# Optimization experiments

Measured on AMD Instinct MI355X. Metric: run time of the kernel, lower is better.

Reference implementation:

```python
import jax, jax.numpy as jnp
import numpy as np

D_MODEL = 256
N_BINS = 11
# standard KNRM kernels: exact-match bin (mu=1, sigma=1e-3) + 10 soft bins
MUS = jnp.array([1.0, 0.9, 0.7, 0.5, 0.3, 0.1, -0.1, -0.3, -0.5, -0.7, -0.9], dtype=jnp.float32)
SIGMAS = jnp.array([1e-3] + [0.1] * 10, dtype=jnp.float32)


def _l2norm(x, eps=1e-10):
    # F.normalize(p=2, eps=1e-10): x / max(||x||, eps)
    n = jnp.sqrt(jnp.sum(x * x, axis=-1, keepdims=True))
    return x / jnp.maximum(n, eps)


def setup_inputs() -> dict:
    key = jax.random.key(0)
    ks = jax.random.split(key, 10)
    B, NB, Q, T, D = 64, 8, 32, 256, D_MODEL
    return {
        "word_atten": jax.random.uniform(ks[0], (B, NB, Q), dtype=jnp.float32),
        "hq": jax.random.normal(ks[1], (B, NB, Q, D), dtype=jnp.float32),
        "can": jax.random.normal(ks[2], (B, T, D), dtype=jnp.float32),
        "rep": jax.random.normal(ks[3], (B, NB, D), dtype=jnp.float32),
        "rep_cur": jax.random.normal(ks[4], (B, D), dtype=jnp.float32),
        "mask_hq": jnp.ones((B, NB, Q), dtype=jnp.float32),
        "mask_can": jnp.ones((B, T), dtype=jnp.float32),
        "mask_session": jnp.ones((B, NB), dtype=jnp.float32),
        "W_dense": jax.random.normal(ks[5], (N_BINS, 1), dtype=jnp.float32) * 0.3,
        "b_dense": jnp.zeros((1,), dtype=jnp.float32),
        "W_att": jax.random.normal(ks[6], (D, D), dtype=jnp.float32) * (1.0 / np.sqrt(D)),
        "b_att": jnp.zeros((D,), dtype=jnp.float32),
    }


def reference(word_atten, hq, can, rep, rep_cur, mask_hq, mask_can, mask_session,
              W_dense, b_dense, W_att, b_att):
    # cosine-similarity matrix: [B, NB, Q, T]
    hq_n = _l2norm(hq)
    can_n = _l2norm(can)
    matrix = jnp.einsum("bnqd,btd->bnqt", hq_n, can_n)

    # Gaussian kernel soft-binning: expand to [B, NB, Q, T, N_BINS]
    diff = matrix[..., None] - MUS  # broadcast over bins
    kern = jnp.exp(-(diff * diff) / (2.0 * SIGMAS * SIGMAS))
    kern = kern * mask_can[:, None, None, :, None]  # mask doc tokens
    pooling_sum = jnp.sum(kern, axis=3)  # [B, NB, Q, N_BINS]

    log_pool = jnp.log(jnp.clip(pooling_sum, 1e-10)) * 0.01
    log_pool = log_pool * mask_hq[..., None] * word_atten[..., None]
    pooled = jnp.sum(log_pool, axis=2)  # [B, NB, N_BINS]

    pooled = pooled * mask_session[..., None]

    # attention over session blocks (AttendAttention): scaled dot with projected current rep
    q = rep_cur @ W_att + b_att  # [B, D]
    scores = jnp.einsum("bnd,bd->bn", rep, q) / np.sqrt(D_MODEL).astype(np.float32)
    scores = jnp.where(mask_session > 0, scores, -1e9)
    attn = jax.nn.softmax(scores, axis=-1)  # [B, NB]

    score = jnp.tanh(pooled @ W_dense + b_dense).squeeze(-1)  # [B, NB]
    return jnp.sum(score * attn, axis=1)  # [B]
```

## Files before the change

kernel.cpp:

```cpp
#include <hip/hip_runtime.h>

#define B_ 64
#define NB_ 8
#define Q_ 32
#define T_ 256
#define D_ 256
#define NBINS 11

typedef __attribute__((ext_vector_type(8))) short bf16x8;
typedef __attribute__((ext_vector_type(4))) float f32x4;
typedef unsigned short ushort_t;
typedef unsigned int uint_t;

__device__ inline ushort_t bf16_rnd(float f) {
  uint_t u = __float_as_uint(f);
  return (ushort_t)((u + 0x8000u) >> 16);
}
__device__ inline uint_t pack2(ushort_t a, ushort_t b) {
  return (uint_t)a | ((uint_t)b << 16);
}

__global__ __launch_bounds__(256) void pool_kernel(
    const float* __restrict__ hq, const float* __restrict__ can,
    const float* __restrict__ mask_can, float* __restrict__ psum) {
  __shared__ __align__(16) ushort_t can_hi[32 * 264];
  __shared__ __align__(16) ushort_t can_lo[32 * 264];
  float* partial = (float*)can_hi;

  const float mus[NBINS] = {1.0f, 0.9f, 0.7f, 0.5f, 0.3f, 0.1f,
                            -0.1f, -0.3f, -0.5f, -0.7f, -0.9f};
  const float nis2[NBINS] = {-5.0e5f, -50.f, -50.f, -50.f, -50.f, -50.f,
                             -50.f, -50.f, -50.f, -50.f, -50.f};

  int i = blockIdx.x;
  int b = i & 63;
  int nb = (i >> 6) & 7;
  int th = i >> 9;
  int outb = b * NB_ + nb;
  int tid = threadIdx.x;
  int wv = tid >> 6, lane = tid & 63;
  int lq = lane & 15, lk = lane >> 4;
  int mtile = wv >> 1, ntile = wv & 1;

  const float* hq_base = hq + (size_t)outb * (Q_ * D_);
  const float* can_base = can + (size_t)b * (T_ * D_);
  const float* maskcan_b = mask_can + b * T_;

  const float* arow = hq_base + (size_t)(mtile * 16 + lq) * D_;
  float sumsq = 0.f;
#pragma unroll
  for (int kk = 0; kk < 8; kk++) {
    const float* p = arow + kk * 32 + lk * 8;
    float4 x = reinterpret_cast<const float4*>(p)[0];
    float4 y = reinterpret_cast<const float4*>(p)[1];
    sumsq += x.x * x.x + x.y * x.y + x.z * x.z + x.w * x.w +
             y.x * y.x + y.y * y.y + y.z * y.z + y.w * y.w;
  }
  sumsq += __shfl_xor(sumsq, 16);
  sumsq += __shfl_xor(sumsq, 32);
  float ainv = 1.0f / fmaxf(sqrtf(sumsq), 1e-10f);

  bf16x8 a_hi[8], a_lo[8];
#pragma unroll
  for (int kk = 0; kk < 8; kk++) {
    const float* p = arow + kk * 32 + lk * 8;
    float4 x = reinterpret_cast<const float4*>(p)[0];
    float4 y = reinterpret_cast<const float4*>(p)[1];
    float v[8] = {x.x, x.y, x.z, x.w, y.x, y.y, y.z, y.w};
    union { bf16x8 v8; ushort_t u[8]; } H, L;
#pragma unroll
    for (int j = 0; j < 8; j++) {
      float s = v[j] * ainv;
      ushort_t h = bf16_rnd(s);
      float hf = __uint_as_float(((uint_t)h) << 16);
      H.u[j] = h;
      L.u[j] = bf16_rnd(s - hf);
    }
    a_hi[kk] = H.v8;
    a_lo[kk] = L.v8;
  }

  float binacc[4][NBINS];
#pragma unroll
  for (int r = 0; r < 4; r++)
#pragma unroll
    for (int j = 0; j < NBINS; j++) binacc[r][j] = 0.0f;

  for (int ch = 0; ch < 4; ch++) {
    __syncthreads();
#pragma unroll
    for (int it = 0; it < 4; it++) {
      int flat = it * 2048 + tid * 8;
      int row = flat >> 8, col = flat & 255;
      int trow = th * 128 + ch * 32 + row;
      const float* src = can_base + (size_t)trow * D_ + col;
      float4 x = reinterpret_cast<const float4*>(src)[0];
      float4 y = reinterpret_cast<const float4*>(src)[1];
      float s = x.x * x.x + x.y * x.y + x.z * x.z + x.w * x.w +
                y.x * y.x + y.y * y.y + y.z * y.z + y.w * y.w;
      s += __shfl_xor(s, 1);
      s += __shfl_xor(s, 2);
      s += __shfl_xor(s, 4);
      s += __shfl_xor(s, 8);
      s += __shfl_xor(s, 16);
      float inv = 1.0f / fmaxf(sqrtf(s), 1e-10f);
      float v[8] = {x.x, x.y, x.z, x.w, y.x, y.y, y.z, y.w};
      ushort_t h[8], l[8];
#pragma unroll
      for (int j = 0; j < 8; j++) {
        float sv = v[j] * inv;
        h[j] = bf16_rnd(sv);
        float hf = __uint_as_float(((uint_t)h[j]) << 16);
        l[j] = bf16_rnd(sv - hf);
      }
      uint4 ph = {pack2(h[0], h[1]), pack2(h[2], h[3]), pack2(h[4], h[5]),
                  pack2(h[6], h[7])};
      uint4 pl = {pack2(l[0], l[1]), pack2(l[2], l[3]), pack2(l[4], l[5]),
                  pack2(l[6], l[7])};
      *reinterpret_cast<uint4*>(&can_hi[row * 264 + col]) = ph;
      *reinterpret_cast<uint4*>(&can_lo[row * 264 + col]) = pl;
    }
    __syncthreads();

    f32x4 acc = {0.f, 0.f, 0.f, 0.f};
    const ushort_t* Bhi = &can_hi[(ntile * 16 + lq) * 264];
    const ushort_t* Blo = &can_lo[(ntile * 16 + lq) * 264];
#pragma unroll
    for (int kk = 0; kk < 8; kk++) {
      int off = kk * 32 + lk * 8;
      bf16x8 bh = *reinterpret_cast<const bf16x8*>(Bhi + off);
      bf16x8 bl = *reinterpret_cast<const bf16x8*>(Blo + off);
      acc = __builtin_amdgcn_mfma_f32_16x16x32_bf16(a_hi[kk], bh, acc, 0, 0, 0);
      acc = __builtin_amdgcn_mfma_f32_16x16x32_bf16(a_lo[kk], bh, acc, 0, 0, 0);
      acc = __builtin_amdgcn_mfma_f32_16x16x32_bf16(a_hi[kk], bl, acc, 0, 0, 0);
    }

    int t0 = th * 128 + ch * 32 + ntile * 16 + lq;
    float mk = maskcan_b[t0];
#pragma unroll
    for (int r = 0; r < 4; r++) {
      float v0 = acc[r];
#pragma unroll
      for (int j = 0; j < NBINS; j++) {
        float d0 = v0 - mus[j];
        binacc[r][j] += mk * __expf(d0 * d0 * nis2[j]);
      }
    }
  }

  __syncthreads();

#pragma unroll
  for (int r = 0; r < 4; r++)
#pragma unroll
    for (int j = 0; j < NBINS; j++) {
      float v = binacc[r][j];
      v += __shfl_xor(v, 1);
      v += __shfl_xor(v, 2);
      v += __shfl_xor(v, 4);
      v += __shfl_xor(v, 8);
      binacc[r][j] = v;
    }
  if (lq == 0) {
#pragma unroll
    for (int r = 0; r < 4; r++)
#pragma unroll
      for (int j = 0; j < NBINS; j++)
        partial[(wv * 16 + lk * 4 + r) * NBINS + j] = binacc[r][j];
  }
  __syncthreads();

  float* dst = &psum[(size_t)(outb * 2 + th) * (Q_ * NBINS)];
  for (int idx = tid; idx < Q_ * NBINS; idx += 256) {
    int q = idx / NBINS;
    int j = idx - q * NBINS;
    int mt = q >> 4, lr = q & 15;
    dst[idx] = partial[((2 * mt) * 16 + lr) * NBINS + j] +
               partial[((2 * mt + 1) * 16 + lr) * NBINS + j];
  }
}

__global__ __launch_bounds__(256) void final_kernel(
    const float* __restrict__ rep, const float* __restrict__ rep_cur,
    const float* __restrict__ mask_session, const float* __restrict__ W_dense,
    const float* __restrict__ b_dense, const float* __restrict__ W_att,
    const float* __restrict__ b_att, const float* __restrict__ word_atten,
    const float* __restrict__ mask_hq, const float* __restrict__ psum,
    float* __restrict__ out) {
  __shared__ float lp[NB_ * Q_ * NBINS];
  __shared__ float pooled_sm[NB_ * NBINS];
  __shared__ float qproj[D_];
  __shared__ float scores_sm[NB_];
  int b = blockIdx.x, tid = threadIdx.x;

  {
    int nb = tid >> 5, q = tid & 31;
    int outb = b * NB_ + nb;
    float wa = word_atten[outb * Q_ + q] * mask_hq[outb * Q_ + q];
    const float* p0 = &psum[(size_t)(outb * 2 + 0) * (Q_ * NBINS) + q * NBINS];
    const float* p1 = &psum[(size_t)(outb * 2 + 1) * (Q_ * NBINS) + q * NBINS];
#pragma unroll
    for (int j = 0; j < NBINS; j++) {
      float s = p0[j] + p1[j];
      lp[(nb * Q_ + q) * NBINS + j] = logf(fmaxf(s, 1e-10f)) * 0.01f * wa;
    }
  }

  const float* rc = rep_cur + b * D_;
  float acc = b_att[tid];
  for (int k = 0; k < D_; k++) acc += rc[k] * W_att[k * D_ + tid];
  qproj[tid] = acc;
  __syncthreads();

  if (tid < NB_ * NBINS) {
    int nb = tid / NBINS, j = tid - nb * NBINS;
    float s = 0.f;
#pragma unroll
    for (int q = 0; q < Q_; q++) s += lp[(nb * Q_ + q) * NBINS + j];
    pooled_sm[nb * NBINS + j] = s;
  }

  int wv = tid >> 6, lane = tid & 63;
  for (int nn = wv; nn < NB_; nn += 4) {
    const float* rp = rep + ((size_t)b * NB_ + nn) * D_;
    float4 r4 = reinterpret_cast<const float4*>(rp)[lane];
    float4 q4 = *reinterpret_cast<float4*>(&qproj[lane * 4]);
    float s = r4.x * q4.x + r4.y * q4.y + r4.z * q4.z + r4.w * q4.w;
#pragma unroll
    for (int off = 32; off > 0; off >>= 1) s += __shfl_down(s, off);
    if (lane == 0) scores_sm[nn] = s * 0.0625f;
  }
  __syncthreads();

  if (tid == 0) {
    float sc[NB_];
    float mx = -1e30f;
    for (int nn = 0; nn < NB_; nn++) {
      float s = (mask_session[b * NB_ + nn] > 0.f) ? scores_sm[nn] : -1e9f;
      sc[nn] = s;
      mx = fmaxf(mx, s);
    }
    float den = 0.f;
    for (int nn = 0; nn < NB_; nn++) {
      sc[nn] = __expf(sc[nn] - mx);
      den += sc[nn];
    }
    float res = 0.f;
    for (int nn = 0; nn < NB_; nn++) {
      float ms = mask_session[b * NB_ + nn];
      float pw = b_dense[0];
      for (int j = 0; j < NBINS; j++)
        pw += pooled_sm[nn * NBINS + j] * ms * W_dense[j];
      res += tanhf(pw) * (sc[nn] / den);
    }
    out[b] = res;
  }
}

extern "C" void kernel_launch(void* const* d_in, const int* in_sizes, int n_in,
                              void* d_out, int out_size, void* d_ws,
                              size_t ws_size, hipStream_t stream) {
  const float* word_atten = (const float*)d_in[0];
  const float* hq = (const float*)d_in[1];
  const float* can = (const float*)d_in[2];
  const float* rep = (const float*)d_in[3];
  const float* rep_cur = (const float*)d_in[4];
  const float* mask_hq = (const float*)d_in[5];
  const float* mask_can = (const float*)d_in[6];
  const float* mask_session = (const float*)d_in[7];
  const float* W_dense = (const float*)d_in[8];
  const float* b_dense = (const float*)d_in[9];
  const float* W_att = (const float*)d_in[10];
  const float* b_att = (const float*)d_in[11];
  float* out = (float*)d_out;

  float* psum = (float*)d_ws;

  hipLaunchKernelGGL(pool_kernel, dim3(1024), dim3(256), 0, stream, hq, can,
                     mask_can, psum);
  hipLaunchKernelGGL(final_kernel, dim3(B_), dim3(256), 0, stream, rep,
                     rep_cur, mask_session, W_dense, b_dense, W_att, b_att,
                     word_atten, mask_hq, psum, out);
}
```

Before: 151.6 us.

## Precompute normalized bf16 hi/lo operand tiles in separate kernel, pipeline pool MFMA loop

Adds a split_kernel that normalizes can and hq once and writes bf16 hi/lo halves to workspace, already arranged in the MFMA fragment layout. Previously each pool block re-normalized and re-split the can rows, and that work was repeated for every nb. pool_kernel now loads fragments straight from global memory with no shared staging and no barriers. It uses 512 blocks that each cover all T, and overlaps the next tile's loads and MFMAs with the exp binning of the previous tile. The cost is an extra launch, a round trip of the converted data through global memory, and more registers, capped by launch_bounds(256,2).

```diff
diff --git a/kernel.cpp b/kernel.cpp
--- a/kernel.cpp
+++ b/kernel.cpp
@@ -12,6 +12,12 @@
 typedef unsigned short ushort_t;
 typedef unsigned int uint_t;
 
+#define CANH_OFF 0u
+#define CANL_OFF 8388608u
+#define HQH_OFF 16777216u
+#define HQL_OFF 25165824u
+#define PSUM_OFF 33554432u
+
 __device__ inline ushort_t bf16_rnd(float f) {
   uint_t u = __float_as_uint(f);
   return (ushort_t)((u + 0x8000u) >> 16);
@@ -20,12 +26,80 @@
   return (uint_t)a | ((uint_t)b << 16);
 }
 
-__global__ __launch_bounds__(256) void pool_kernel(
-    const float* __restrict__ hq, const float* __restrict__ can,
+__global__ __launch_bounds__(256) void split_kernel(
+    const float* __restrict__ can, const float* __restrict__ hq,
+    uint4* __restrict__ canH, uint4* __restrict__ canL,
+    uint4* __restrict__ hqH, uint4* __restrict__ hqL) {
+  __shared__ __align__(16) ushort_t sm_hi[32 * 264];
+  __shared__ __align__(16) ushort_t sm_lo[32 * 264];
+  int blk = blockIdx.x;
+  int tid = threadIdx.x;
+  const float* src;
+  uint4 *dH, *dL;
+  int tilebase;
+  if (blk < 512) {
+    int b = blk >> 3, ch = blk & 7;
+    src = can + ((size_t)b * T_ + ch * 32) * D_;
+    tilebase = b * 16 + ch * 2;
+    dH = canH;
+    dL = canL;
+  } else {
+    int outb = blk - 512;
+    src = hq + (size_t)outb * Q_ * D_;
+    tilebase = outb * 2;
+    dH = hqH;
+    dL = hqL;
+  }
+#pragma unroll
+  for (int it = 0; it < 4; it++) {
+    int flat = it * 2048 + tid * 8;
+    int row = flat >> 8, col = flat & 255;
+    const float* p = src + row * D_ + col;
+    float4 x = reinterpret_cast<const float4*>(p)[0];
+    float4 y = reinterpret_cast<const float4*>(p)[1];
+    float s = x.x * x.x + x.y * x.y + x.z * x.z + x.w * x.w +
+              y.x * y.x + y.y * y.y + y.z * y.z + y.w * y.w;
+    s += __shfl_xor(s, 1);
+    s += __shfl_xor(s, 2);
+    s += __shfl_xor(s, 4);
+    s += __shfl_xor(s, 8);
+    s += __shfl_xor(s, 16);
+    float inv = 1.0f / fmaxf(sqrtf(s), 1e-10f);
+    float v[8] = {x.x, x.y, x.z, x.w, y.x, y.y, y.z, y.w};
+    ushort_t h[8], l[8];
+#pragma unroll
+    for (int j = 0; j < 8; j++) {
+      float sv = v[j] * inv;
+      h[j] = bf16_rnd(sv);
+      float hf = __uint_as_float(((uint_t)h[j]) << 16);
+      l[j] = bf16_rnd(sv - hf);
+    }
+    uint4 ph = {pack2(h[0], h[1]), pack2(h[2], h[3]), pack2(h[4], h[5]),
+                pack2(h[6], h[7])};
+    uint4 pl = {pack2(l[0], l[1]), pack2(l[2], l[3]), pack2(l[4], l[5]),
+                pack2(l[6], l[7])};
+    *reinterpret_cast<uint4*>(&sm_hi[row * 264 + col]) = ph;
+    *reinterpret_cast<uint4*>(&sm_lo[row * 264 + col]) = pl;
+  }
+  __syncthreads();
+  int wv = tid >> 6, lane = tid & 63;
+  int tl = wv >> 1, part = wv & 1;
+  int lq = lane & 15, lk = lane >> 4;
+  const ushort_t* smp = part ? sm_lo : sm_hi;
+  uint4* dst = part ? dL : dH;
+#pragma unroll
+  for (int kk = 0; kk < 8; kk++) {
+    const ushort_t* a = &smp[(tl * 16 + lq) * 264 + kk * 32 + lk * 8];
+    dst[((size_t)(tilebase + tl) * 8 + kk) * 64 + lane] =
+        *reinterpret_cast<const uint4*>(a);
+  }
+}
+
+__global__ __launch_bounds__(256, 2) void pool_kernel(
+    const uint4* __restrict__ canH, const uint4* __restrict__ canL,
+    const uint4* __restrict__ hqH, const uint4* __restrict__ hqL,
     const float* __restrict__ mask_can, float* __restrict__ psum) {
-  __shared__ __align__(16) ushort_t can_hi[32 * 264];
-  __shared__ __align__(16) ushort_t can_lo[32 * 264];
-  float* partial = (float*)can_hi;
+  __shared__ float partial[4 * 16 * NBINS];
 
   const float mus[NBINS] = {1.0f, 0.9f, 0.7f, 0.5f, 0.3f, 0.1f,
                             -0.1f, -0.3f, -0.5f, -0.7f, -0.9f};
@@ -34,50 +108,21 @@
 
   int i = blockIdx.x;
   int b = i & 63;
-  int nb = (i >> 6) & 7;
-  int th = i >> 9;
+  int nb = i >> 6;
   int outb = b * NB_ + nb;
   int tid = threadIdx.x;
   int wv = tid >> 6, lane = tid & 63;
   int lq = lane & 15, lk = lane >> 4;
-  int mtile = wv >> 1, ntile = wv & 1;
-
-  const float* hq_base = hq + (size_t)outb * (Q_ * D_);
-  const float* can_base = can + (size_t)b * (T_ * D_);
-  const float* maskcan_b = mask_can + b * T_;
-
-  const float* arow = hq_base + (size_t)(mtile * 16 + lq) * D_;
-  float sumsq = 0.f;
-#pragma unroll
-  for (int kk = 0; kk < 8; kk++) {
-    const float* p = arow + kk * 32 + lk * 8;
-    float4 x = reinterpret_cast<const float4*>(p)[0];
-    float4 y = reinterpret_cast<const float4*>(p)[1];
-    sumsq += x.x * x.x + x.y * x.y + x.z * x.z + x.w * x.w +
-             y.x * y.x + y.y * y.y + y.z * y.z + y.w * y.w;
-  }
-  sumsq += __shfl_xor(sumsq, 16);
-  sumsq += __shfl_xor(sumsq, 32);
-  float ainv = 1.0f / fmaxf(sqrtf(sumsq), 1e-10f);
-
-  bf16x8 a_hi[8], a_lo[8];
-#pragma unroll
-  for (int kk = 0; kk < 8; kk++) {
-    const float* p = arow + kk * 32 + lk * 8;
-    float4 x = reinterpret_cast<const float4*>(p)[0];
-    float4 y = reinterpret_cast<const float4*>(p)[1];
-    float v[8] = {x.x, x.y, x.z, x.w, y.x, y.y, y.z, y.w};
-    union { bf16x8 v8; ushort_t u[8]; } H, L;
-#pragma unroll
-    for (int j = 0; j < 8; j++) {
-      float s = v[j] * ainv;
-      ushort_t h = bf16_rnd(s);
-      float hf = __uint_as_float(((uint_t)h) << 16);
-      H.u[j] = h;
-      L.u[j] = bf16_rnd(s - hf);
-    }
-    a_hi[kk] = H.v8;
-    a_lo[kk] = L.v8;
+  int mtile = wv & 1, tq = wv >> 1;
+
+  bf16x8 ah[8], al[8];
+  {
+    size_t abase = (size_t)(outb * 2 + mtile) * 8 * 64 + lane;
+#pragma unroll
+    for (int kk = 0; kk < 8; kk++) {
+      ah[kk] = *reinterpret_cast<const bf16x8*>(&hqH[abase + kk * 64]);
+      al[kk] = *reinterpret_cast<const bf16x8*>(&hqL[abase + kk * 64]);
+    }
   }
 
   float binacc[4][NBINS];
@@ -86,69 +131,62 @@
 #pragma unroll
     for (int j = 0; j < NBINS; j++) binacc[r][j] = 0.0f;
 
-  for (int ch = 0; ch < 4; ch++) {
-    __syncthreads();
-#pragma unroll
-    for (int it = 0; it < 4; it++) {
-      int flat = it * 2048 + tid * 8;
-      int row = flat >> 8, col = flat & 255;
-      int trow = th * 128 + ch * 32 + row;
-      const float* src = can_base + (size_t)trow * D_ + col;
-      float4 x = reinterpret_cast<const float4*>(src)[0];
-      float4 y = reinterpret_cast<const float4*>(src)[1];
-      float s = x.x * x.x + x.y * x.y + x.z * x.z + x.w * x.w +
-                y.x * y.x + y.y * y.y + y.z * y.z + y.w * y.w;
-      s += __shfl_xor(s, 1);
-      s += __shfl_xor(s, 2);
-      s += __shfl_xor(s, 4);
-      s += __shfl_xor(s, 8);
-      s += __shfl_xor(s, 16);
-      float inv = 1.0f / fmaxf(sqrtf(s), 1e-10f);
-      float v[8] = {x.x, x.y, x.z, x.w, y.x, y.y, y.z, y.w};
-      ushort_t h[8], l[8];
-#pragma unroll
-      for (int j = 0; j < 8; j++) {
-        float sv = v[j] * inv;
-        h[j] = bf16_rnd(sv);
-        float hf = __uint_as_float(((uint_t)h[j]) << 16);
-        l[j] = bf16_rnd(sv - hf);
-      }
-      uint4 ph = {pack2(h[0], h[1]), pack2(h[2], h[3]), pack2(h[4], h[5]),
-                  pack2(h[6], h[7])};
-      uint4 pl = {pack2(l[0], l[1]), pack2(l[2], l[3]), pack2(l[4], l[5]),
-                  pack2(l[6], l[7])};
-      *reinterpret_cast<uint4*>(&can_hi[row * 264 + col]) = ph;
-      *reinterpret_cast<uint4*>(&can_lo[row * 264 + col]) = pl;
-    }
-    __syncthreads();
-
+  f32x4 accPrev;
+  float mkPrev = 0.0f;
+
+  {
+    int tt = tq * 8;
+    size_t bbase = (size_t)(b * 16 + tt) * 8 * 64 + lane;
     f32x4 acc = {0.f, 0.f, 0.f, 0.f};
-    const ushort_t* Bhi = &can_hi[(ntile * 16 + lq) * 264];
-    const ushort_t* Blo = &can_lo[(ntile * 16 + lq) * 264];
 #pragma unroll
     for (int kk = 0; kk < 8; kk++) {
-      int off = kk * 32 + lk * 8;
-      bf16x8 bh = *reinterpret_cast<const bf16x8*>(Bhi + off);
-      bf16x8 bl = *reinterpret_cast<const bf16x8*>(Blo + off);
-      acc = __builtin_amdgcn_mfma_f32_16x16x32_bf16(a_hi[kk], bh, acc, 0, 0, 0);
-      acc = __builtin_amdgcn_mfma_f32_16x16x32_bf16(a_lo[kk], bh, acc, 0, 0, 0);
-      acc = __builtin_amdgcn_mfma_f32_16x16x32_bf16(a_hi[kk], bl, acc, 0, 0, 0);
-    }
-
-    int t0 = th * 128 + ch * 32 + ntile * 16 + lq;
-    float mk = maskcan_b[t0];
+      bf16x8 bh = *reinterpret_cast<const bf16x8*>(&canH[bbase + kk * 64]);
+      bf16x8 bl = *reinterpret_cast<const bf16x8*>(&canL[bbase + kk * 64]);
+      acc = __builtin_amdgcn_mfma_f32_16x16x32_bf16(ah[kk], bh, acc, 0, 0, 0);
+      acc = __builtin_amdgcn_mfma_f32_16x16x32_bf16(al[kk], bh, acc, 0, 0, 0);
+      acc = __builtin_amdgcn_mfma_f32_16x16x32_bf16(ah[kk], bl, acc, 0, 0, 0);
+    }
+    accPrev = acc;
+    mkPrev = mask_can[b * T_ + tt * 16 + lq];
+  }
+
+  for (int ti = 1; ti < 8; ti++) {
+    int tt = tq * 8 + ti;
+    size_t bbase = (size_t)(b * 16 + tt) * 8 * 64 + lane;
+    bf16x8 bh[8], bl[8];
+#pragma unroll
+    for (int kk = 0; kk < 8; kk++) {
+      bh[kk] = *reinterpret_cast<const bf16x8*>(&canH[bbase + kk * 64]);
+      bl[kk] = *reinterpret_cast<const bf16x8*>(&canL[bbase + kk * 64]);
+    }
 #pragma unroll
     for (int r = 0; r < 4; r++) {
-      float v0 = acc[r];
+      float v0 = accPrev[r];
 #pragma unroll
       for (int j = 0; j < NBINS; j++) {
         float d0 = v0 - mus[j];
-        binacc[r][j] += mk * __expf(d0 * d0 * nis2[j]);
+        binacc[r][j] += mkPrev * __expf(d0 * d0 * nis2[j]);
       }
     }
-  }
-
-  __syncthreads();
+    f32x4 acc = {0.f, 0.f, 0.f, 0.f};
+#pragma unroll
+    for (int kk = 0; kk < 8; kk++) {
+      acc = __builtin_amdgcn_mfma_f32_16x16x32_bf16(ah[kk], bh[kk], acc, 0, 0, 0);
+      acc = __builtin_amdgcn_mfma_f32_16x16x32_bf16(al[kk], bh[kk], acc, 0, 0, 0);
+      acc = __builtin_amdgcn_mfma_f32_16x16x32_bf16(ah[kk], bl[kk], acc, 0, 0, 0);
+    }
+    accPrev = acc;
+    mkPrev = mask_can[b * T_ + tt * 16 + lq];
+  }
+#pragma unroll
+  for (int r = 0; r < 4; r++) {
+    float v0 = accPrev[r];
+#pragma unroll
+    for (int j = 0; j < NBINS; j++) {
+      float d0 = v0 - mus[j];
+      binacc[r][j] += mkPrev * __expf(d0 * d0 * nis2[j]);
+    }
+  }
 
 #pragma unroll
   for (int r = 0; r < 4; r++)
@@ -170,13 +208,13 @@
   }
   __syncthreads();
 
-  float* dst = &psum[(size_t)(outb * 2 + th) * (Q_ * NBINS)];
+  float* dst = &psum[(size_t)outb * (Q_ * NBINS)];
   for (int idx = tid; idx < Q_ * NBINS; idx += 256) {
     int q = idx / NBINS;
     int j = idx - q * NBINS;
-    int mt = q >> 4, lr = q & 15;
-    dst[idx] = partial[((2 * mt) * 16 + lr) * NBINS + j] +
-               partial[((2 * mt + 1) * 16 + lr) * NBINS + j];
+    int m = q >> 4, r16 = q & 15;
+    dst[idx] = partial[(m * 16 + r16) * NBINS + j] +
+               partial[((2 + m) * 16 + r16) * NBINS + j];
   }
 }
 
@@ -197,13 +235,10 @@
     int nb = tid >> 5, q = tid & 31;
     int outb = b * NB_ + nb;
     float wa = word_atten[outb * Q_ + q] * mask_hq[outb * Q_ + q];
-    const float* p0 = &psum[(size_t)(outb * 2 + 0) * (Q_ * NBINS) + q * NBINS];
-    const float* p1 = &psum[(size_t)(outb * 2 + 1) * (Q_ * NBINS) + q * NBINS];
-#pragma unroll
-    for (int j = 0; j < NBINS; j++) {
-      float s = p0[j] + p1[j];
-      lp[(nb * Q_ + q) * NBINS + j] = logf(fmaxf(s, 1e-10f)) * 0.01f * wa;
-    }
+    const float* ps = &psum[(size_t)outb * (Q_ * NBINS) + q * NBINS];
+#pragma unroll
+    for (int j = 0; j < NBINS; j++)
+      lp[(nb * Q_ + q) * NBINS + j] = logf(fmaxf(ps[j], 1e-10f)) * 0.01f * wa;
   }
 
   const float* rc = rep_cur + b * D_;
@@ -274,10 +309,17 @@
   const float* b_att = (const float*)d_in[11];
   float* out = (float*)d_out;
 
-  float* psum = (float*)d_ws;
-
-  hipLaunchKernelGGL(pool_kernel, dim3(1024), dim3(256), 0, stream, hq, can,
-                     mask_can, psum);
+  char* ws = (char*)d_ws;
+  uint4* canH = (uint4*)(ws + CANH_OFF);
+  uint4* canL = (uint4*)(ws + CANL_OFF);
+  uint4* hqH = (uint4*)(ws + HQH_OFF);
+  uint4* hqL = (uint4*)(ws + HQL_OFF);
+  float* psum = (float*)(ws + PSUM_OFF);
+
+  hipLaunchKernelGGL(split_kernel, dim3(1024), dim3(256), 0, stream, can, hq,
+                     canH, canL, hqH, hqL);
+  hipLaunchKernelGGL(pool_kernel, dim3(B_ * NB_), dim3(256), 0, stream, canH,
+                     canL, hqH, hqL, mask_can, psum);
   hipLaunchKernelGGL(final_kernel, dim3(B_), dim3(256), 0, stream, rep,
                      rep_cur, mask_session, W_dense, b_dense, W_att, b_att,
                      word_atten, mask_hq, psum, out);
```

Measured after the change: 132.5 us. -12.6%, faster.
